# Kernel tuning notes

Measured on AMD Instinct MI355X. Metric: run time of the kernel, lower is better.

Reference implementation:

```python
import jax, jax.numpy as jnp
import numpy as np
from jax import lax

BN_EPS = 1e-5


def fake_quant(x, bits):
    # trax-style symmetric fixed-point fake quant, UPWARD (round-half-up) rounding,
    # range [-1, 1 - 2^-(bits-1)], straight-through estimator for grads.
    s = jnp.asarray(2.0 ** (bits - 1), x.dtype)
    q = jnp.clip(jnp.floor(x * s + 0.5), -s, s - 1.0) / s
    return x + lax.stop_gradient(q - x)


def conv1d(x, w):
    # x: [N, C, L], w: [O, I, K], padding=1, stride=1
    return lax.conv_general_dilated(x, w, window_strides=(1,), padding=((1, 1),),
                                    dimension_numbers=('NCH', 'OIH', 'NCH'))


def setup_inputs() -> dict:
    key = jax.random.key(0)
    ks = jax.random.split(key, 9)
    B, L = 16, 524288
    return {
        'x': jax.random.normal(ks[0], (B, 4, L), jnp.float32),
        'w1': jax.random.normal(ks[1], (8, 4, 3), jnp.float32) * 0.3,
        'b1': jax.random.normal(ks[2], (8,), jnp.float32) * 0.1,
        'gamma': jax.random.uniform(ks[3], (8,), jnp.float32, 0.5, 1.5),
        'beta': jax.random.normal(ks[4], (8,), jnp.float32) * 0.1,
        'bn_mean': jax.random.normal(ks[5], (8,), jnp.float32) * 0.1,
        'bn_var': jax.random.uniform(ks[6], (8,), jnp.float32, 0.5, 1.5),
        'w2': jax.random.normal(ks[7], (2, 8, 3), jnp.float32) * 0.3,
        'b2': jax.random.normal(ks[8], (2,), jnp.float32) * 0.1,
    }


def reference(x, w1, b1, gamma, beta, bn_mean, bn_var, w2, b2):
    BW_F, BW_W, BW_B = 8, 8, 8
    # input fake-quant (activation_post_process)
    x = fake_quant(x, BW_F)
    # ConvBn1d: fold BN into conv weight/bias, fake-quant folded params
    sf = gamma * lax.rsqrt(bn_var + BN_EPS)                    # [8]
    wq = fake_quant(w1 * sf[:, None, None], BW_W)              # [8,4,3]
    bq = fake_quant((b1 - bn_mean) * sf + beta, BW_B)          # [8]
    y = conv1d(x, wq) + bq[None, :, None]                      # [B,8,L]
    y = fake_quant(y, BW_F)
    # Conv1d (quantized weight + bias, no BN, no ReLU since act=False)
    z = conv1d(y, fake_quant(w2, BW_W)) + fake_quant(b2, BW_B)[None, :, None]
    z = fake_quant(z, BW_F)                                    # [B,2,L]
    return z
```

## Files before the change

### kernel.cpp

```cpp
#include <hip/hip_runtime.h>
#include <hip/hip_bf16.h>


#define T 8

__device__ __forceinline__ float q128(float v) {
    float t = floorf(fmaf(v, 128.0f, 0.5f));
    return fminf(fmaxf(t, -128.0f), 127.0f);
}

__device__ __forceinline__ float fq8(float v) { return q128(v) * 0.0078125f; }

__global__ __launch_bounds__(256) void fused_qconv_kernel(
    const float* __restrict__ x,
    const float* __restrict__ w1, const float* __restrict__ b1,
    const float* __restrict__ gamma, const float* __restrict__ beta,
    const float* __restrict__ bn_mean, const float* __restrict__ bn_var,
    const float* __restrict__ w2, const float* __restrict__ b2,
    float* __restrict__ out,
    int L, int chunksPerRow)
{
    __shared__ float s_cw[8][20];
    __shared__ float s_b2[2];

    const int t = threadIdx.x;
    if (t < 162) {
        if (t < 160) {
            const int c = t / 20, j = t - c * 20;
            float v;
            if (j < 12) {
                float sf = gamma[c] * (1.0f / sqrtf(bn_var[c] + 1e-5f));
                v = fq8(w1[c * 12 + j] * sf);
            } else if (j == 12) {
                float sf = gamma[c] * (1.0f / sqrtf(bn_var[c] + 1e-5f));
                v = fmaf(fq8((b1[c] - bn_mean[c]) * sf + beta[c]), 128.0f, 0.5f);
            } else if (j < 16) {
                v = fq8(w2[c * 3 + (j - 13)]);
            } else if (j < 19) {
                v = fq8(w2[24 + c * 3 + (j - 16)]);
            } else {
                v = 0.0f;
            }
            s_cw[c][j] = v;
        } else {
            s_b2[t - 160] = fmaf(fq8(b2[t - 160]), 128.0f, 0.5f);
        }
    }
    __syncthreads();

    const int pc = blockIdx.x * blockDim.x + t;
    if (pc >= chunksPerRow) return;
    const int n = blockIdx.y;
    const int pos0 = pc * T;
    const bool le = (pos0 == 0);
    const bool re = (pos0 + T == L);

    float X[4][12];
    const float* xb = x + (size_t)(n * 4) * (size_t)L + (unsigned)pos0;
#pragma unroll
    for (int i = 0; i < 4; ++i) {
        const float* xr = xb + (unsigned)(i * L);
        float4 a = *(const float4*)(xr);
        float4 b = *(const float4*)(xr + 4);
        X[i][2] = q128(a.x); X[i][3] = q128(a.y); X[i][4] = q128(a.z); X[i][5] = q128(a.w);
        X[i][6] = q128(b.x); X[i][7] = q128(b.y); X[i][8] = q128(b.z); X[i][9] = q128(b.w);
        if (!le) {
            float4 h = *(const float4*)(xr - 4);
            X[i][0] = q128(h.z); X[i][1] = q128(h.w);
        } else { X[i][0] = 0.0f; X[i][1] = 0.0f; }
        if (!re) {
            float4 h = *(const float4*)(xr + 8);
            X[i][10] = q128(h.x); X[i][11] = q128(h.y);
        } else { X[i][10] = 0.0f; X[i][11] = 0.0f; }
    }

    float acc[2][T];
    {
        const float a0 = s_b2[0], a1 = s_b2[1];
#pragma unroll
        for (int j = 0; j < T; ++j) { acc[0][j] = a0; acc[1][j] = a1; }
    }

#pragma unroll
    for (int c = 0; c < 8; ++c) {
        const float4 cw0 = *(const float4*)&s_cw[c][0];
        const float4 cw1 = *(const float4*)&s_cw[c][4];
        const float4 cw2 = *(const float4*)&s_cw[c][8];
        const float4 cw3 = *(const float4*)&s_cw[c][12];
        const float4 cw4 = *(const float4*)&s_cw[c][16];
        const float w00 = cw0.x, w01 = cw0.y, w02 = cw0.z;
        const float w10 = cw0.w, w11 = cw1.x, w12 = cw1.y;
        const float w20 = cw1.z, w21 = cw1.w, w22 = cw2.x;
        const float w30 = cw2.y, w31 = cw2.z, w32 = cw2.w;
        const float bc  = cw3.x;
        const float u0 = cw3.y, u1 = cw3.z, u2 = cw3.w;
        const float v0 = cw4.x, v1 = cw4.y, v2 = cw4.z;

#pragma unroll
        for (int p = 0; p < T + 2; ++p) {
            float v = bc;
            v = fmaf(X[0][p], w00, v); v = fmaf(X[0][p + 1], w01, v); v = fmaf(X[0][p + 2], w02, v);
            v = fmaf(X[1][p], w10, v); v = fmaf(X[1][p + 1], w11, v); v = fmaf(X[1][p + 2], w12, v);
            v = fmaf(X[2][p], w20, v); v = fmaf(X[2][p + 1], w21, v); v = fmaf(X[2][p + 2], w22, v);
            v = fmaf(X[3][p], w30, v); v = fmaf(X[3][p + 1], w31, v); v = fmaf(X[3][p + 2], w32, v);
            float Y = fminf(fmaxf(floorf(v), -128.0f), 127.0f);
            if (p == 0     && le) Y = 0.0f;
            if (p == T + 1 && re) Y = 0.0f;
            if (p < T) {
                acc[0][p] = fmaf(Y, u0, acc[0][p]);
                acc[1][p] = fmaf(Y, v0, acc[1][p]);
            }
            if (p >= 1 && p - 1 < T) {
                acc[0][p - 1] = fmaf(Y, u1, acc[0][p - 1]);
                acc[1][p - 1] = fmaf(Y, v1, acc[1][p - 1]);
            }
            if (p >= 2) {
                acc[0][p - 2] = fmaf(Y, u2, acc[0][p - 2]);
                acc[1][p - 2] = fmaf(Y, v2, acc[1][p - 2]);
            }
        }
    }

    float* ob = out + (size_t)(n * 2) * (size_t)L + (unsigned)pos0;
#pragma unroll
    for (int o = 0; o < 2; ++o) {
        float4 r0, r1;
        r0.x = fminf(fmaxf(floorf(acc[o][0]), -128.0f), 127.0f) * 0.0078125f;
        r0.y = fminf(fmaxf(floorf(acc[o][1]), -128.0f), 127.0f) * 0.0078125f;
        r0.z = fminf(fmaxf(floorf(acc[o][2]), -128.0f), 127.0f) * 0.0078125f;
        r0.w = fminf(fmaxf(floorf(acc[o][3]), -128.0f), 127.0f) * 0.0078125f;
        r1.x = fminf(fmaxf(floorf(acc[o][4]), -128.0f), 127.0f) * 0.0078125f;
        r1.y = fminf(fmaxf(floorf(acc[o][5]), -128.0f), 127.0f) * 0.0078125f;
        r1.z = fminf(fmaxf(floorf(acc[o][6]), -128.0f), 127.0f) * 0.0078125f;
        r1.w = fminf(fmaxf(floorf(acc[o][7]), -128.0f), 127.0f) * 0.0078125f;
        *(float4*)(ob + (size_t)o * (size_t)L)     = r0;
        *(float4*)(ob + (size_t)o * (size_t)L + 4) = r1;
    }
}

extern "C" void kernel_launch(void* const* d_in, const int* in_sizes, int n_in,
                              void* d_out, int out_size, void* d_ws, size_t ws_size,
                              hipStream_t stream) {
    const float* x       = (const float*)d_in[0];
    const float* w1      = (const float*)d_in[1];
    const float* b1      = (const float*)d_in[2];
    const float* gamma   = (const float*)d_in[3];
    const float* beta    = (const float*)d_in[4];
    const float* bn_mean = (const float*)d_in[5];
    const float* bn_var  = (const float*)d_in[6];
    const float* w2      = (const float*)d_in[7];
    const float* b2      = (const float*)d_in[8];
    float* out = (float*)d_out;

    const int B = 16;
    const int L = in_sizes[0] / (B * 4);
    const int chunksPerRow = L / T;
    const int block = 256;
    const int gridX = (chunksPerRow + block - 1) / block;

    fused_qconv_kernel<<<dim3(gridX, B), block, 0, stream>>>(
        x, w1, b1, gamma, beta, bn_mean, bn_var, w2, b2, out,
        L, chunksPerRow);
}
```

Before: 240.8 us.

## Process four batch rows per thread with software-prefetched next-row loads

Each thread now handles the same position chunk across four batch rows in sequence, loading the next row's main input while the current row is computed. The halo loads are made unconditional by redirecting them to in-bounds addresses at the edges, and launch bounds request four blocks per SM. The grid shrinks by a factor of four, the weight setup in shared memory is amortized over more work, and the bounds check is removed on the assumption that L divides evenly by 2048. The aim is to hide memory latency in a bandwidth-bound kernel. The cost is higher register pressure and fewer blocks in flight.

```diff
diff --git a/kernel.cpp b/kernel.cpp
--- a/kernel.cpp
+++ b/kernel.cpp
@@ -11,14 +11,14 @@
 
 __device__ __forceinline__ float fq8(float v) { return q128(v) * 0.0078125f; }
 
-__global__ __launch_bounds__(256) void fused_qconv_kernel(
+__global__ __launch_bounds__(256, 4) void fused_qconv_kernel(
     const float* __restrict__ x,
     const float* __restrict__ w1, const float* __restrict__ b1,
     const float* __restrict__ gamma, const float* __restrict__ beta,
     const float* __restrict__ bn_mean, const float* __restrict__ bn_var,
     const float* __restrict__ w2, const float* __restrict__ b2,
     float* __restrict__ out,
-    int L, int chunksPerRow)
+    int L)
 {
     __shared__ float s_cw[8][20];
     __shared__ float s_b2[2];
@@ -48,93 +48,126 @@
     }
     __syncthreads();
 
-    const int pc = blockIdx.x * blockDim.x + t;
-    if (pc >= chunksPerRow) return;
-    const int n = blockIdx.y;
+    const int pc   = blockIdx.x * 256 + t;
     const int pos0 = pc * T;
     const bool le = (pos0 == 0);
     const bool re = (pos0 + T == L);
+    const int n0 = blockIdx.y * 4;
 
-    float X[4][12];
-    const float* xb = x + (size_t)(n * 4) * (size_t)L + (unsigned)pos0;
+    const unsigned chStride  = (unsigned)L;
+    const unsigned batStride = (unsigned)(4 * L);
+    const unsigned base0 = (unsigned)(n0 * 4) * (unsigned)L + (unsigned)pos0;
+
+    float4 m[4][2];
 #pragma unroll
     for (int i = 0; i < 4; ++i) {
-        const float* xr = xb + (unsigned)(i * L);
-        float4 a = *(const float4*)(xr);
-        float4 b = *(const float4*)(xr + 4);
-        X[i][2] = q128(a.x); X[i][3] = q128(a.y); X[i][4] = q128(a.z); X[i][5] = q128(a.w);
-        X[i][6] = q128(b.x); X[i][7] = q128(b.y); X[i][8] = q128(b.z); X[i][9] = q128(b.w);
-        if (!le) {
-            float4 h = *(const float4*)(xr - 4);
-            X[i][0] = q128(h.z); X[i][1] = q128(h.w);
-        } else { X[i][0] = 0.0f; X[i][1] = 0.0f; }
-        if (!re) {
-            float4 h = *(const float4*)(xr + 8);
-            X[i][10] = q128(h.x); X[i][11] = q128(h.y);
-        } else { X[i][10] = 0.0f; X[i][11] = 0.0f; }
-    }
-
-    float acc[2][T];
-    {
-        const float a0 = s_b2[0], a1 = s_b2[1];
-#pragma unroll
-        for (int j = 0; j < T; ++j) { acc[0][j] = a0; acc[1][j] = a1; }
+        const float* bi = x + base0 + (unsigned)i * chStride;
+        m[i][0] = *(const float4*)(bi);
+        m[i][1] = *(const float4*)(bi + 4);
     }
 
 #pragma unroll
-    for (int c = 0; c < 8; ++c) {
-        const float4 cw0 = *(const float4*)&s_cw[c][0];
-        const float4 cw1 = *(const float4*)&s_cw[c][4];
-        const float4 cw2 = *(const float4*)&s_cw[c][8];
-        const float4 cw3 = *(const float4*)&s_cw[c][12];
-        const float4 cw4 = *(const float4*)&s_cw[c][16];
-        const float w00 = cw0.x, w01 = cw0.y, w02 = cw0.z;
-        const float w10 = cw0.w, w11 = cw1.x, w12 = cw1.y;
-        const float w20 = cw1.z, w21 = cw1.w, w22 = cw2.x;
-        const float w30 = cw2.y, w31 = cw2.z, w32 = cw2.w;
-        const float bc  = cw3.x;
-        const float u0 = cw3.y, u1 = cw3.z, u2 = cw3.w;
-        const float v0 = cw4.x, v1 = cw4.y, v2 = cw4.z;
+    for (int j = 0; j < 4; ++j) {
+        const unsigned bj = base0 + (unsigned)j * batStride;
+
+        float4 hl[4], hr[4];
+#pragma unroll
+        for (int i = 0; i < 4; ++i) {
+            const float* bi = x + bj + (unsigned)i * chStride;
+            hl[i] = *(const float4*)(le ? bi : bi - 4);
+            hr[i] = *(const float4*)(re ? bi + 4 : bi + 8);
+        }
+
+        float X[4][12];
+#pragma unroll
+        for (int i = 0; i < 4; ++i) {
+            X[i][2] = q128(m[i][0].x); X[i][3] = q128(m[i][0].y);
+            X[i][4] = q128(m[i][0].z); X[i][5] = q128(m[i][0].w);
+            X[i][6] = q128(m[i][1].x); X[i][7] = q128(m[i][1].y);
+            X[i][8] = q128(m[i][1].z); X[i][9] = q128(m[i][1].w);
+        }
+
+        if (j < 3) {
+            const unsigned bn = base0 + (unsigned)(j + 1) * batStride;
+#pragma unroll
+            for (int i = 0; i < 4; ++i) {
+                const float* bi = x + bn + (unsigned)i * chStride;
+                m[i][0] = *(const float4*)(bi);
+                m[i][1] = *(const float4*)(bi + 4);
+            }
+        }
 
 #pragma unroll
-        for (int p = 0; p < T + 2; ++p) {
-            float v = bc;
-            v = fmaf(X[0][p], w00, v); v = fmaf(X[0][p + 1], w01, v); v = fmaf(X[0][p + 2], w02, v);
-            v = fmaf(X[1][p], w10, v); v = fmaf(X[1][p + 1], w11, v); v = fmaf(X[1][p + 2], w12, v);
-            v = fmaf(X[2][p], w20, v); v = fmaf(X[2][p + 1], w21, v); v = fmaf(X[2][p + 2], w22, v);
-            v = fmaf(X[3][p], w30, v); v = fmaf(X[3][p + 1], w31, v); v = fmaf(X[3][p + 2], w32, v);
-            float Y = fminf(fmaxf(floorf(v), -128.0f), 127.0f);
-            if (p == 0     && le) Y = 0.0f;
-            if (p == T + 1 && re) Y = 0.0f;
-            if (p < T) {
-                acc[0][p] = fmaf(Y, u0, acc[0][p]);
-                acc[1][p] = fmaf(Y, v0, acc[1][p]);
-            }
-            if (p >= 1 && p - 1 < T) {
-                acc[0][p - 1] = fmaf(Y, u1, acc[0][p - 1]);
-                acc[1][p - 1] = fmaf(Y, v1, acc[1][p - 1]);
-            }
-            if (p >= 2) {
-                acc[0][p - 2] = fmaf(Y, u2, acc[0][p - 2]);
-                acc[1][p - 2] = fmaf(Y, v2, acc[1][p - 2]);
+        for (int i = 0; i < 4; ++i) {
+            X[i][0]  = le ? 0.0f : q128(hl[i].z);
+            X[i][1]  = le ? 0.0f : q128(hl[i].w);
+            X[i][10] = re ? 0.0f : q128(hr[i].x);
+            X[i][11] = re ? 0.0f : q128(hr[i].y);
+        }
+
+        float acc[2][T];
+        {
+            const float a0 = s_b2[0], a1 = s_b2[1];
+#pragma unroll
+            for (int q = 0; q < T; ++q) { acc[0][q] = a0; acc[1][q] = a1; }
+        }
+
+#pragma unroll
+        for (int c = 0; c < 8; ++c) {
+            const float4 cw0 = *(const float4*)&s_cw[c][0];
+            const float4 cw1 = *(const float4*)&s_cw[c][4];
+            const float4 cw2 = *(const float4*)&s_cw[c][8];
+            const float4 cw3 = *(const float4*)&s_cw[c][12];
+            const float4 cw4 = *(const float4*)&s_cw[c][16];
+            const float w00 = cw0.x, w01 = cw0.y, w02 = cw0.z;
+            const float w10 = cw0.w, w11 = cw1.x, w12 = cw1.y;
+            const float w20 = cw1.z, w21 = cw1.w, w22 = cw2.x;
+            const float w30 = cw2.y, w31 = cw2.z, w32 = cw2.w;
+            const float bc  = cw3.x;
+            const float u0 = cw3.y, u1 = cw3.z, u2 = cw3.w;
+            const float v0 = cw4.x, v1 = cw4.y, v2 = cw4.z;
+
+#pragma unroll
+            for (int p = 0; p < T + 2; ++p) {
+                float v = bc;
+                v = fmaf(X[0][p], w00, v); v = fmaf(X[0][p+1], w01, v); v = fmaf(X[0][p+2], w02, v);
+                v = fmaf(X[1][p], w10, v); v = fmaf(X[1][p+1], w11, v); v = fmaf(X[1][p+2], w12, v);
+                v = fmaf(X[2][p], w20, v); v = fmaf(X[2][p+1], w21, v); v = fmaf(X[2][p+2], w22, v);
+                v = fmaf(X[3][p], w30, v); v = fmaf(X[3][p+1], w31, v); v = fmaf(X[3][p+2], w32, v);
+                float Y = fminf(fmaxf(floorf(v), -128.0f), 127.0f);
+                if (p == 0     && le) Y = 0.0f;
+                if (p == T + 1 && re) Y = 0.0f;
+                if (p < T) {
+                    acc[0][p] = fmaf(Y, u0, acc[0][p]);
+                    acc[1][p] = fmaf(Y, v0, acc[1][p]);
+                }
+                if (p >= 1 && p - 1 < T) {
+                    acc[0][p-1] = fmaf(Y, u1, acc[0][p-1]);
+                    acc[1][p-1] = fmaf(Y, v1, acc[1][p-1]);
+                }
+                if (p >= 2) {
+                    acc[0][p-2] = fmaf(Y, u2, acc[0][p-2]);
+                    acc[1][p-2] = fmaf(Y, v2, acc[1][p-2]);
+                }
             }
         }
-    }
 
-    float* ob = out + (size_t)(n * 2) * (size_t)L + (unsigned)pos0;
+        const int n = n0 + j;
+        float* ob = out + (unsigned)(n * 2) * (unsigned)L + (unsigned)pos0;
 #pragma unroll
-    for (int o = 0; o < 2; ++o) {
-        float4 r0, r1;
-        r0.x = fminf(fmaxf(floorf(acc[o][0]), -128.0f), 127.0f) * 0.0078125f;
-        r0.y = fminf(fmaxf(floorf(acc[o][1]), -128.0f), 127.0f) * 0.0078125f;
-        r0.z = fminf(fmaxf(floorf(acc[o][2]), -128.0f), 127.0f) * 0.0078125f;
-        r0.w = fminf(fmaxf(floorf(acc[o][3]), -128.0f), 127.0f) * 0.0078125f;
-        r1.x = fminf(fmaxf(floorf(acc[o][4]), -128.0f), 127.0f) * 0.0078125f;
-        r1.y = fminf(fmaxf(floorf(acc[o][5]), -128.0f), 127.0f) * 0.0078125f;
-        r1.z = fminf(fmaxf(floorf(acc[o][6]), -128.0f), 127.0f) * 0.0078125f;
-        r1.w = fminf(fmaxf(floorf(acc[o][7]), -128.0f), 127.0f) * 0.0078125f;
-        *(float4*)(ob + (size_t)o * (size_t)L)     = r0;
-        *(float4*)(ob + (size_t)o * (size_t)L + 4) = r1;
+        for (int o = 0; o < 2; ++o) {
+            float4 r0, r1;
+            r0.x = fminf(fmaxf(floorf(acc[o][0]), -128.0f), 127.0f) * 0.0078125f;
+            r0.y = fminf(fmaxf(floorf(acc[o][1]), -128.0f), 127.0f) * 0.0078125f;
+            r0.z = fminf(fmaxf(floorf(acc[o][2]), -128.0f), 127.0f) * 0.0078125f;
+            r0.w = fminf(fmaxf(floorf(acc[o][3]), -128.0f), 127.0f) * 0.0078125f;
+            r1.x = fminf(fmaxf(floorf(acc[o][4]), -128.0f), 127.0f) * 0.0078125f;
+            r1.y = fminf(fmaxf(floorf(acc[o][5]), -128.0f), 127.0f) * 0.0078125f;
+            r1.z = fminf(fmaxf(floorf(acc[o][6]), -128.0f), 127.0f) * 0.0078125f;
+            r1.w = fminf(fmaxf(floorf(acc[o][7]), -128.0f), 127.0f) * 0.0078125f;
+            *(float4*)(ob + (size_t)o * (size_t)L)     = r0;
+            *(float4*)(ob + (size_t)o * (size_t)L + 4) = r1;
+        }
     }
 }
 
@@ -154,11 +187,9 @@
 
     const int B = 16;
     const int L = in_sizes[0] / (B * 4);
-    const int chunksPerRow = L / T;
-    const int block = 256;
-    const int gridX = (chunksPerRow + block - 1) / block;
+    const int gridX = (L / T) / 256;
+    const int gridY = B / 4;
 
-    fused_qconv_kernel<<<dim3(gridX, B), block, 0, stream>>>(
-        x, w1, b1, gamma, beta, bn_mean, bn_var, w2, b2, out,
-        L, chunksPerRow);
+    fused_qconv_kernel<<<dim3(gridX, gridY), 256, 0, stream>>>(
+        x, w1, b1, gamma, beta, bn_mean, bn_var, w2, b2, out, L);
 }
```

New measurement: 265.2 us. +10.1%, slower.

## Process multiple chunks per thread with register double-buffered prefetch

Applied to the files above, without the earlier changes.

Each thread now handles 8 consecutive chunks strided across the block and issues the global loads for the next chunk before computing the current one, using a two-slot register buffer. This amortizes the per-block weight setup in shared memory and hides memory latency behind the conv arithmetic. Halo loads become float2 instead of float4. Launch bounds request 2 blocks per CU; the larger register footprint may reduce occupancy, and the grid shrinks 8x, which assumes L divides evenly by 16384.

```diff
diff --git a/kernel.cpp b/kernel.cpp
--- a/kernel.cpp
+++ b/kernel.cpp
@@ -3,6 +3,7 @@
 
 
 #define T 8
+#define CHUNKS 8
 
 __device__ __forceinline__ float q128(float v) {
     float t = floorf(fmaf(v, 128.0f, 0.5f));
@@ -11,14 +12,31 @@
 
 __device__ __forceinline__ float fq8(float v) { return q128(v) * 0.0078125f; }
 
-__global__ __launch_bounds__(256) void fused_qconv_kernel(
+#define ISSUE_CHUNK(JJ)                                                    \
+    {                                                                      \
+        const int  bb    = (JJ) & 1;                                       \
+        const int  pp    = blockBase + ((JJ) * 256 + t) * T;               \
+        const float* basep = x + rowBase + (unsigned)pp;                   \
+        const bool pll = (pp == 0);                                        \
+        const bool prr = (pp + T == L);                                    \
+        _Pragma("unroll")                                                  \
+        for (int i = 0; i < 4; ++i) {                                      \
+            const float* bi = basep + (unsigned)i * (unsigned)L;           \
+            m[bb][i][0] = *(const float4*)(bi);                            \
+            m[bb][i][1] = *(const float4*)(bi + 4);                        \
+            hl[bb][i]   = *(const float2*)(pll ? bi : bi - 2);             \
+            hr[bb][i]   = *(const float2*)(prr ? bi : bi + T);             \
+        }                                                                  \
+    }
+
+__global__ __launch_bounds__(256, 2) void fused_qconv_kernel(
     const float* __restrict__ x,
     const float* __restrict__ w1, const float* __restrict__ b1,
     const float* __restrict__ gamma, const float* __restrict__ beta,
     const float* __restrict__ bn_mean, const float* __restrict__ bn_var,
     const float* __restrict__ w2, const float* __restrict__ b2,
     float* __restrict__ out,
-    int L, int chunksPerRow)
+    int L)
 {
     __shared__ float s_cw[8][20];
     __shared__ float s_b2[2];
@@ -48,93 +66,99 @@
     }
     __syncthreads();
 
-    const int pc = blockIdx.x * blockDim.x + t;
-    if (pc >= chunksPerRow) return;
     const int n = blockIdx.y;
-    const int pos0 = pc * T;
-    const bool le = (pos0 == 0);
-    const bool re = (pos0 + T == L);
+    const int blockBase = blockIdx.x * (256 * CHUNKS * T);
+    const unsigned rowBase = (unsigned)(n * 4) * (unsigned)L;
 
-    float X[4][12];
-    const float* xb = x + (size_t)(n * 4) * (size_t)L + (unsigned)pos0;
-#pragma unroll
-    for (int i = 0; i < 4; ++i) {
-        const float* xr = xb + (unsigned)(i * L);
-        float4 a = *(const float4*)(xr);
-        float4 b = *(const float4*)(xr + 4);
-        X[i][2] = q128(a.x); X[i][3] = q128(a.y); X[i][4] = q128(a.z); X[i][5] = q128(a.w);
-        X[i][6] = q128(b.x); X[i][7] = q128(b.y); X[i][8] = q128(b.z); X[i][9] = q128(b.w);
-        if (!le) {
-            float4 h = *(const float4*)(xr - 4);
-            X[i][0] = q128(h.z); X[i][1] = q128(h.w);
-        } else { X[i][0] = 0.0f; X[i][1] = 0.0f; }
-        if (!re) {
-            float4 h = *(const float4*)(xr + 8);
-            X[i][10] = q128(h.x); X[i][11] = q128(h.y);
-        } else { X[i][10] = 0.0f; X[i][11] = 0.0f; }
-    }
+    float4 m[2][4][2];
+    float2 hl[2][4], hr[2][4];
 
-    float acc[2][T];
-    {
-        const float a0 = s_b2[0], a1 = s_b2[1];
-#pragma unroll
-        for (int j = 0; j < T; ++j) { acc[0][j] = a0; acc[1][j] = a1; }
-    }
+    ISSUE_CHUNK(0);
 
 #pragma unroll
-    for (int c = 0; c < 8; ++c) {
-        const float4 cw0 = *(const float4*)&s_cw[c][0];
-        const float4 cw1 = *(const float4*)&s_cw[c][4];
-        const float4 cw2 = *(const float4*)&s_cw[c][8];
-        const float4 cw3 = *(const float4*)&s_cw[c][12];
-        const float4 cw4 = *(const float4*)&s_cw[c][16];
-        const float w00 = cw0.x, w01 = cw0.y, w02 = cw0.z;
-        const float w10 = cw0.w, w11 = cw1.x, w12 = cw1.y;
-        const float w20 = cw1.z, w21 = cw1.w, w22 = cw2.x;
-        const float w30 = cw2.y, w31 = cw2.z, w32 = cw2.w;
-        const float bc  = cw3.x;
-        const float u0 = cw3.y, u1 = cw3.z, u2 = cw3.w;
-        const float v0 = cw4.x, v1 = cw4.y, v2 = cw4.z;
+    for (int j = 0; j < CHUNKS; ++j) {
+        const int  b  = j & 1;
+        const int  p  = blockBase + (j * 256 + t) * T;
+        const bool pl = (p == 0);
+        const bool pr = (p + T == L);
+
+        float X[4][12];
+#pragma unroll
+        for (int i = 0; i < 4; ++i) {
+            X[i][2] = q128(m[b][i][0].x); X[i][3] = q128(m[b][i][0].y);
+            X[i][4] = q128(m[b][i][0].z); X[i][5] = q128(m[b][i][0].w);
+            X[i][6] = q128(m[b][i][1].x); X[i][7] = q128(m[b][i][1].y);
+            X[i][8] = q128(m[b][i][1].z); X[i][9] = q128(m[b][i][1].w);
+            X[i][0]  = pl ? 0.0f : q128(hl[b][i].x);
+            X[i][1]  = pl ? 0.0f : q128(hl[b][i].y);
+            X[i][10] = pr ? 0.0f : q128(hr[b][i].x);
+            X[i][11] = pr ? 0.0f : q128(hr[b][i].y);
+        }
+
+        if (j + 1 < CHUNKS) ISSUE_CHUNK(j + 1);
+
+        float acc[2][T];
+        {
+            const float a0 = s_b2[0], a1 = s_b2[1];
+#pragma unroll
+            for (int q = 0; q < T; ++q) { acc[0][q] = a0; acc[1][q] = a1; }
+        }
 
 #pragma unroll
-        for (int p = 0; p < T + 2; ++p) {
-            float v = bc;
-            v = fmaf(X[0][p], w00, v); v = fmaf(X[0][p + 1], w01, v); v = fmaf(X[0][p + 2], w02, v);
-            v = fmaf(X[1][p], w10, v); v = fmaf(X[1][p + 1], w11, v); v = fmaf(X[1][p + 2], w12, v);
-            v = fmaf(X[2][p], w20, v); v = fmaf(X[2][p + 1], w21, v); v = fmaf(X[2][p + 2], w22, v);
-            v = fmaf(X[3][p], w30, v); v = fmaf(X[3][p + 1], w31, v); v = fmaf(X[3][p + 2], w32, v);
-            float Y = fminf(fmaxf(floorf(v), -128.0f), 127.0f);
-            if (p == 0     && le) Y = 0.0f;
-            if (p == T + 1 && re) Y = 0.0f;
-            if (p < T) {
-                acc[0][p] = fmaf(Y, u0, acc[0][p]);
-                acc[1][p] = fmaf(Y, v0, acc[1][p]);
-            }
-            if (p >= 1 && p - 1 < T) {
-                acc[0][p - 1] = fmaf(Y, u1, acc[0][p - 1]);
-                acc[1][p - 1] = fmaf(Y, v1, acc[1][p - 1]);
-            }
-            if (p >= 2) {
-                acc[0][p - 2] = fmaf(Y, u2, acc[0][p - 2]);
-                acc[1][p - 2] = fmaf(Y, v2, acc[1][p - 2]);
+        for (int c = 0; c < 8; ++c) {
+            const float4 cw0 = *(const float4*)&s_cw[c][0];
+            const float4 cw1 = *(const float4*)&s_cw[c][4];
+            const float4 cw2 = *(const float4*)&s_cw[c][8];
+            const float4 cw3 = *(const float4*)&s_cw[c][12];
+            const float4 cw4 = *(const float4*)&s_cw[c][16];
+            const float w00 = cw0.x, w01 = cw0.y, w02 = cw0.z;
+            const float w10 = cw0.w, w11 = cw1.x, w12 = cw1.y;
+            const float w20 = cw1.z, w21 = cw1.w, w22 = cw2.x;
+            const float w30 = cw2.y, w31 = cw2.z, w32 = cw2.w;
+            const float bc  = cw3.x;
+            const float u0 = cw3.y, u1 = cw3.z, u2 = cw3.w;
+            const float v0 = cw4.x, v1 = cw4.y, v2 = cw4.z;
+
+#pragma unroll
+            for (int pp = 0; pp < T + 2; ++pp) {
+                float v = bc;
+                v = fmaf(X[0][pp], w00, v); v = fmaf(X[0][pp+1], w01, v); v = fmaf(X[0][pp+2], w02, v);
+                v = fmaf(X[1][pp], w10, v); v = fmaf(X[1][pp+1], w11, v); v = fmaf(X[1][pp+2], w12, v);
+                v = fmaf(X[2][pp], w20, v); v = fmaf(X[2][pp+1], w21, v); v = fmaf(X[2][pp+2], w22, v);
+                v = fmaf(X[3][pp], w30, v); v = fmaf(X[3][pp+1], w31, v); v = fmaf(X[3][pp+2], w32, v);
+                float Y = fminf(fmaxf(floorf(v), -128.0f), 127.0f);
+                if (pp == 0     && pl) Y = 0.0f;
+                if (pp == T + 1 && pr) Y = 0.0f;
+                if (pp < T) {
+                    acc[0][pp] = fmaf(Y, u0, acc[0][pp]);
+                    acc[1][pp] = fmaf(Y, v0, acc[1][pp]);
+                }
+                if (pp >= 1 && pp - 1 < T) {
+                    acc[0][pp-1] = fmaf(Y, u1, acc[0][pp-1]);
+                    acc[1][pp-1] = fmaf(Y, v1, acc[1][pp-1]);
+                }
+                if (pp >= 2) {
+                    acc[0][pp-2] = fmaf(Y, u2, acc[0][pp-2]);
+                    acc[1][pp-2] = fmaf(Y, v2, acc[1][pp-2]);
+                }
             }
         }
-    }
 
-    float* ob = out + (size_t)(n * 2) * (size_t)L + (unsigned)pos0;
+        float* ob = out + (unsigned)(n * 2) * (unsigned)L + (unsigned)p;
 #pragma unroll
-    for (int o = 0; o < 2; ++o) {
-        float4 r0, r1;
-        r0.x = fminf(fmaxf(floorf(acc[o][0]), -128.0f), 127.0f) * 0.0078125f;
-        r0.y = fminf(fmaxf(floorf(acc[o][1]), -128.0f), 127.0f) * 0.0078125f;
-        r0.z = fminf(fmaxf(floorf(acc[o][2]), -128.0f), 127.0f) * 0.0078125f;
-        r0.w = fminf(fmaxf(floorf(acc[o][3]), -128.0f), 127.0f) * 0.0078125f;
-        r1.x = fminf(fmaxf(floorf(acc[o][4]), -128.0f), 127.0f) * 0.0078125f;
-        r1.y = fminf(fmaxf(floorf(acc[o][5]), -128.0f), 127.0f) * 0.0078125f;
-        r1.z = fminf(fmaxf(floorf(acc[o][6]), -128.0f), 127.0f) * 0.0078125f;
-        r1.w = fminf(fmaxf(floorf(acc[o][7]), -128.0f), 127.0f) * 0.0078125f;
-        *(float4*)(ob + (size_t)o * (size_t)L)     = r0;
-        *(float4*)(ob + (size_t)o * (size_t)L + 4) = r1;
+        for (int o = 0; o < 2; ++o) {
+            float4 r0, r1;
+            r0.x = fminf(fmaxf(floorf(acc[o][0]), -128.0f), 127.0f) * 0.0078125f;
+            r0.y = fminf(fmaxf(floorf(acc[o][1]), -128.0f), 127.0f) * 0.0078125f;
+            r0.z = fminf(fmaxf(floorf(acc[o][2]), -128.0f), 127.0f) * 0.0078125f;
+            r0.w = fminf(fmaxf(floorf(acc[o][3]), -128.0f), 127.0f) * 0.0078125f;
+            r1.x = fminf(fmaxf(floorf(acc[o][4]), -128.0f), 127.0f) * 0.0078125f;
+            r1.y = fminf(fmaxf(floorf(acc[o][5]), -128.0f), 127.0f) * 0.0078125f;
+            r1.z = fminf(fmaxf(floorf(acc[o][6]), -128.0f), 127.0f) * 0.0078125f;
+            r1.w = fminf(fmaxf(floorf(acc[o][7]), -128.0f), 127.0f) * 0.0078125f;
+            *(float4*)(ob + (unsigned)o * (unsigned)L)     = r0;
+            *(float4*)(ob + (unsigned)o * (unsigned)L + 4) = r1;
+        }
     }
 }
 
@@ -154,11 +178,9 @@
 
     const int B = 16;
     const int L = in_sizes[0] / (B * 4);
-    const int chunksPerRow = L / T;
-    const int block = 256;
-    const int gridX = (chunksPerRow + block - 1) / block;
+    const int gridX = L / (256 * CHUNKS * T);
+    const int gridY = B;
 
-    fused_qconv_kernel<<<dim3(gridX, B), block, 0, stream>>>(
-        x, w1, b1, gamma, beta, bn_mean, bn_var, w2, b2, out,
-        L, chunksPerRow);
+    fused_qconv_kernel<<<dim3(gridX, gridY), 256, 0, stream>>>(
+        x, w1, b1, gamma, beta, bn_mean, bn_var, w2, b2, out, L);
 }
```

Result: slower. 306.4 us (+27.2%).

## Split weight folding into a prep kernel and read folded weights from workspace

Applied to the files above, without the earlier changes.

Moves BN folding and weight fake-quantisation out of every block into a separate single-block prep kernel that writes to workspace. The main kernel then reads the weights as uniform global loads instead of computing them and doing a shared-memory barrier. It also loads the halos as unconditional float2 reads with selects, switches address arithmetic to 32-bit, drops the bounds check, and raises the launch-bounds occupancy hint. The trade-offs are an extra kernel launch, and the grid now assumes L is a multiple of 2048.

```diff
diff --git a/kernel.cpp b/kernel.cpp
--- a/kernel.cpp
+++ b/kernel.cpp
@@ -1,5 +1,4 @@
 #include <hip/hip_runtime.h>
-#include <hip/hip_bf16.h>
 
 
 #define T 8
@@ -11,98 +10,91 @@
 
 __device__ __forceinline__ float fq8(float v) { return q128(v) * 0.0078125f; }
 
-__global__ __launch_bounds__(256) void fused_qconv_kernel(
-    const float* __restrict__ x,
+__global__ void prep_weights(
     const float* __restrict__ w1, const float* __restrict__ b1,
     const float* __restrict__ gamma, const float* __restrict__ beta,
     const float* __restrict__ bn_mean, const float* __restrict__ bn_var,
     const float* __restrict__ w2, const float* __restrict__ b2,
+    float* __restrict__ ws)
+{
+    const int t = threadIdx.x;
+    if (t < 160) {
+        const int c = t / 20, j = t - c * 20;
+        float v;
+        if (j < 12) {
+            float sf = gamma[c] * (1.0f / sqrtf(bn_var[c] + 1e-5f));
+            v = fq8(w1[c * 12 + j] * sf);
+        } else if (j == 12) {
+            float sf = gamma[c] * (1.0f / sqrtf(bn_var[c] + 1e-5f));
+            v = fmaf(fq8((b1[c] - bn_mean[c]) * sf + beta[c]), 128.0f, 0.5f);
+        } else if (j < 16) {
+            v = fq8(w2[c * 3 + (j - 13)]);
+        } else if (j < 19) {
+            v = fq8(w2[24 + c * 3 + (j - 16)]);
+        } else {
+            v = 0.0f;
+        }
+        ws[t] = v;
+    } else if (t < 162) {
+        ws[t] = fmaf(fq8(b2[t - 160]), 128.0f, 0.5f);
+    }
+}
+
+__global__ __launch_bounds__(256, 8) void fused_qconv_kernel(
+    const float* __restrict__ x,
+    const float* __restrict__ wsu,
     float* __restrict__ out,
-    int L, int chunksPerRow)
+    int L)
 {
-    __shared__ float s_cw[8][20];
-    __shared__ float s_b2[2];
-
     const int t = threadIdx.x;
-    if (t < 162) {
-        if (t < 160) {
-            const int c = t / 20, j = t - c * 20;
-            float v;
-            if (j < 12) {
-                float sf = gamma[c] * (1.0f / sqrtf(bn_var[c] + 1e-5f));
-                v = fq8(w1[c * 12 + j] * sf);
-            } else if (j == 12) {
-                float sf = gamma[c] * (1.0f / sqrtf(bn_var[c] + 1e-5f));
-                v = fmaf(fq8((b1[c] - bn_mean[c]) * sf + beta[c]), 128.0f, 0.5f);
-            } else if (j < 16) {
-                v = fq8(w2[c * 3 + (j - 13)]);
-            } else if (j < 19) {
-                v = fq8(w2[24 + c * 3 + (j - 16)]);
-            } else {
-                v = 0.0f;
-            }
-            s_cw[c][j] = v;
-        } else {
-            s_b2[t - 160] = fmaf(fq8(b2[t - 160]), 128.0f, 0.5f);
-        }
-    }
-    __syncthreads();
-
-    const int pc = blockIdx.x * blockDim.x + t;
-    if (pc >= chunksPerRow) return;
-    const int n = blockIdx.y;
+    const int pc   = blockIdx.x * 256 + t;
     const int pos0 = pc * T;
+    const int n    = blockIdx.y;
     const bool le = (pos0 == 0);
     const bool re = (pos0 + T == L);
 
     float X[4][12];
-    const float* xb = x + (size_t)(n * 4) * (size_t)L + (unsigned)pos0;
+    const float* xb = x + (unsigned)(n * 4) * (unsigned)L + (unsigned)pos0;
 #pragma unroll
     for (int i = 0; i < 4; ++i) {
         const float* xr = xb + (unsigned)(i * L);
         float4 a = *(const float4*)(xr);
         float4 b = *(const float4*)(xr + 4);
+        float2 hl = *(const float2*)(le ? xr : xr - 2);
+        float2 hr = *(const float2*)(re ? xr : xr + T);
         X[i][2] = q128(a.x); X[i][3] = q128(a.y); X[i][4] = q128(a.z); X[i][5] = q128(a.w);
         X[i][6] = q128(b.x); X[i][7] = q128(b.y); X[i][8] = q128(b.z); X[i][9] = q128(b.w);
-        if (!le) {
-            float4 h = *(const float4*)(xr - 4);
-            X[i][0] = q128(h.z); X[i][1] = q128(h.w);
-        } else { X[i][0] = 0.0f; X[i][1] = 0.0f; }
-        if (!re) {
-            float4 h = *(const float4*)(xr + 8);
-            X[i][10] = q128(h.x); X[i][11] = q128(h.y);
-        } else { X[i][10] = 0.0f; X[i][11] = 0.0f; }
+        X[i][0]  = le ? 0.0f : q128(hl.x);
+        X[i][1]  = le ? 0.0f : q128(hl.y);
+        X[i][10] = re ? 0.0f : q128(hr.x);
+        X[i][11] = re ? 0.0f : q128(hr.y);
     }
 
     float acc[2][T];
     {
-        const float a0 = s_b2[0], a1 = s_b2[1];
+        const float a0 = wsu[160], a1 = wsu[161];
 #pragma unroll
-        for (int j = 0; j < T; ++j) { acc[0][j] = a0; acc[1][j] = a1; }
+        for (int q = 0; q < T; ++q) { acc[0][q] = a0; acc[1][q] = a1; }
     }
 
 #pragma unroll
     for (int c = 0; c < 8; ++c) {
-        const float4 cw0 = *(const float4*)&s_cw[c][0];
-        const float4 cw1 = *(const float4*)&s_cw[c][4];
-        const float4 cw2 = *(const float4*)&s_cw[c][8];
-        const float4 cw3 = *(const float4*)&s_cw[c][12];
-        const float4 cw4 = *(const float4*)&s_cw[c][16];
-        const float w00 = cw0.x, w01 = cw0.y, w02 = cw0.z;
-        const float w10 = cw0.w, w11 = cw1.x, w12 = cw1.y;
-        const float w20 = cw1.z, w21 = cw1.w, w22 = cw2.x;
-        const float w30 = cw2.y, w31 = cw2.z, w32 = cw2.w;
-        const float bc  = cw3.x;
-        const float u0 = cw3.y, u1 = cw3.z, u2 = cw3.w;
-        const float v0 = cw4.x, v1 = cw4.y, v2 = cw4.z;
+        const float* wc = wsu + c * 20;
+        const float w00 = wc[0], w01 = wc[1],  w02 = wc[2];
+        const float w10 = wc[3], w11 = wc[4],  w12 = wc[5];
+        const float w20 = wc[6], w21 = wc[7],  w22 = wc[8];
+        const float w30 = wc[9], w31 = wc[10], w32 = wc[11];
+        const float bc  = wc[12];
+        const float u0 = wc[13], u1 = wc[14], u2 = wc[15];
+        const float v0 = wc[16], v1 = wc[17], v2 = wc[18];
 
 #pragma unroll
         for (int p = 0; p < T + 2; ++p) {
             float v = bc;
-            v = fmaf(X[0][p], w00, v); v = fmaf(X[0][p + 1], w01, v); v = fmaf(X[0][p + 2], w02, v);
-            v = fmaf(X[1][p], w10, v); v = fmaf(X[1][p + 1], w11, v); v = fmaf(X[1][p + 2], w12, v);
-            v = fmaf(X[2][p], w20, v); v = fmaf(X[2][p + 1], w21, v); v = fmaf(X[2][p + 2], w22, v);
-            v = fmaf(X[3][p], w30, v); v = fmaf(X[3][p + 1], w31, v); v = fmaf(X[3][p + 2], w32, v);
+            v = fmaf(X[0][p], w00, v); v = fmaf(X[0][p+1], w01, v); v = fmaf(X[0][p+2], w02, v);
+            v = fmaf(X[1][p], w10, v); v = fmaf(X[1][p+1], w11, v); v = fmaf(X[1][p+2], w12, v);
+            v = fmaf(X[2][p], w20, v); v = fmaf(X[2][p+1], w21, v); v = fmaf(X[2][p+2], w22, v);
+            v = fmaf(X[3][p], w30, v); v = fmaf(X[3][p+1], w31, v); v = fmaf(X[3][p+2], w32, v);
             float Y = fminf(fmaxf(floorf(v), -128.0f), 127.0f);
             if (p == 0     && le) Y = 0.0f;
             if (p == T + 1 && re) Y = 0.0f;
@@ -111,17 +103,17 @@
                 acc[1][p] = fmaf(Y, v0, acc[1][p]);
             }
             if (p >= 1 && p - 1 < T) {
-                acc[0][p - 1] = fmaf(Y, u1, acc[0][p - 1]);
-                acc[1][p - 1] = fmaf(Y, v1, acc[1][p - 1]);
+                acc[0][p-1] = fmaf(Y, u1, acc[0][p-1]);
+                acc[1][p-1] = fmaf(Y, v1, acc[1][p-1]);
             }
             if (p >= 2) {
-                acc[0][p - 2] = fmaf(Y, u2, acc[0][p - 2]);
-                acc[1][p - 2] = fmaf(Y, v2, acc[1][p - 2]);
+                acc[0][p-2] = fmaf(Y, u2, acc[0][p-2]);
+                acc[1][p-2] = fmaf(Y, v2, acc[1][p-2]);
             }
         }
     }
 
-    float* ob = out + (size_t)(n * 2) * (size_t)L + (unsigned)pos0;
+    float* ob = out + (unsigned)(n * 2) * (unsigned)L + (unsigned)pos0;
 #pragma unroll
     for (int o = 0; o < 2; ++o) {
         float4 r0, r1;
@@ -133,8 +125,8 @@
         r1.y = fminf(fmaxf(floorf(acc[o][5]), -128.0f), 127.0f) * 0.0078125f;
         r1.z = fminf(fmaxf(floorf(acc[o][6]), -128.0f), 127.0f) * 0.0078125f;
         r1.w = fminf(fmaxf(floorf(acc[o][7]), -128.0f), 127.0f) * 0.0078125f;
-        *(float4*)(ob + (size_t)o * (size_t)L)     = r0;
-        *(float4*)(ob + (size_t)o * (size_t)L + 4) = r1;
+        *(float4*)(ob + (unsigned)o * (unsigned)L)     = r0;
+        *(float4*)(ob + (unsigned)o * (unsigned)L + 4) = r1;
     }
 }
 
@@ -151,14 +143,14 @@
     const float* w2      = (const float*)d_in[7];
     const float* b2      = (const float*)d_in[8];
     float* out = (float*)d_out;
+    float* ws  = (float*)d_ws;
 
     const int B = 16;
     const int L = in_sizes[0] / (B * 4);
-    const int chunksPerRow = L / T;
-    const int block = 256;
-    const int gridX = (chunksPerRow + block - 1) / block;
+    const int gridX = (L / T) / 256;
+    const int gridY = B;
 
-    fused_qconv_kernel<<<dim3(gridX, B), block, 0, stream>>>(
-        x, w1, b1, gamma, beta, bn_mean, bn_var, w2, b2, out,
-        L, chunksPerRow);
+    prep_weights<<<1, 256, 0, stream>>>(w1, b1, gamma, beta, bn_mean, bn_var,
+                                        w2, b2, ws);
+    fused_qconv_kernel<<<dim3(gridX, gridY), 256, 0, stream>>>(x, ws, out, L);
 }
```

Result: slower. 289.7 us (+20.3%).
